# Kernel optimization log

Hardware: AMD Instinct MI355X
Metric: run time of the kernel (lower is better)

The kernel has to match this reference:

```python
import jax, jax.numpy as jnp
import numpy as np

# ---- config (mirrors init_kwargs) ----
R = 0.15          # ball-query radius
K = 32            # neighbors per ball
SP_STRIDE = 32    # spatial FPS stride
T_KERNEL = 3      # temporal tube length (odd)
T_STRIDE = 2
T_PAD = (1, 1)    # replicate padding
C0, C1 = 64, 128  # mlp_planes


def setup_inputs() -> dict:
    key = jax.random.key(0)
    k1, k2, k3 = jax.random.split(key, 3)
    B, T, N = 4, 32, 4096
    xyzs = jax.random.uniform(k1, (B, T, N, 3), dtype=jnp.float32)
    # 1x1 conv weights (no bias, no BN): conv_d: 4 -> C0, mlp: C0 -> C1
    Wd = jax.random.normal(k2, (C0, 4), dtype=jnp.float32) * (1.0 / np.sqrt(4))
    Wm = jax.random.normal(k3, (C1, C0), dtype=jnp.float32) * (1.0 / np.sqrt(C0))
    return {"xyzs": xyzs, "Wd": Wd, "Wm": Wm}


def _fps(xyz, m):
    """Furthest point sampling. xyz: (G,N,3) -> (G,m) int32, first index = 0."""
    G, N, _ = xyz.shape
    def step(carry, _):
        dist, last = carry                                   # (G,N), (G,)
        p = jnp.take_along_axis(xyz, last[:, None, None], axis=1)  # (G,1,3)
        d = jnp.sum((xyz - p) ** 2, axis=-1)                 # (G,N)
        dist = jnp.minimum(dist, d)
        nxt = jnp.argmax(dist, axis=-1).astype(jnp.int32)
        return (dist, nxt), nxt
    init = (jnp.full((G, N), 1e10, dtype=xyz.dtype), jnp.zeros((G,), jnp.int32))
    _, nxts = jax.lax.scan(step, init, None, length=m - 1)   # (m-1, G)
    return jnp.concatenate([jnp.zeros((G, 1), jnp.int32), jnp.swapaxes(nxts, 0, 1)], axis=1)


def _ball_query(r, k, neighbor_xyz, anchor_xyz):
    """First-k-within-radius, invalid slots filled with first valid (PointNet++ semantics).
    neighbor: (G,N,3), anchor: (G,M,3) -> idx (G,M,k) int32."""
    N = neighbor_xyz.shape[1]
    d2 = jnp.sum((anchor_xyz[:, :, None, :] - neighbor_xyz[:, None, :, :]) ** 2, axis=-1)  # (G,M,N)
    score = jnp.where(d2 < r * r, jnp.arange(N, dtype=jnp.int32), N)
    neg_topk, _ = jax.lax.top_k(-score, k)   # k smallest scores (ascending point index)
    idx = -neg_topk                          # (G,M,k)
    first = idx[..., :1]
    first = jnp.where(first == N, 0, first)
    return jnp.where(idx == N, first, idx)


def _group(pts, idx):
    """pts: (G,N,C), idx: (G,M,k) -> (G,M,k,C)."""
    G, M, k = idx.shape
    flat = jnp.take_along_axis(pts, idx.reshape(G, M * k)[..., None], axis=1)
    return flat.reshape(G, M, k, pts.shape[-1])


def _forward(xyzs, Wd, Wm):
    B, T, N, _ = xyzs.shape
    # replicate temporal padding
    xyz_pad = jnp.concatenate([xyzs[:, :1]] * T_PAD[0] + [xyzs] + [xyzs[:, -1:]] * T_PAD[1], axis=1)
    Tp = T + T_PAD[0] + T_PAD[1]
    half = T_KERNEL // 2
    ts = half + T_STRIDE * np.arange((Tp - T_KERNEL) // T_STRIDE + 1)  # output frame centers
    F = len(ts)
    M = N // SP_STRIDE

    center = xyz_pad[:, ts].reshape(B * F, N, 3)          # (G,N,3)
    anchor_idx = _fps(center, M)                          # (G,M)
    anchor = jnp.take_along_axis(center, anchor_idx[..., None], axis=1)  # (G,M,3)

    feat_sum = None
    for dt in range(-half, half + 1):                     # temporal tube (len 3)
        neigh = xyz_pad[:, ts + dt].reshape(B * F, N, 3)
        idx = _ball_query(R, K, neigh, anchor)            # (G,M,K)
        grouped = _group(neigh, idx)                      # (G,M,K,3)
        disp = grouped - anchor[:, :, None, :]
        tchan = jnp.full(disp.shape[:-1] + (1,), float(dt), dtype=disp.dtype)
        d4 = jnp.concatenate([disp, tchan], axis=-1)      # (G,M,K,4)
        h = jax.nn.relu(jnp.einsum('gmkc,oc->gmko', d4, Wd))   # conv_d + ReLU
        h = jax.nn.relu(jnp.einsum('gmki,oi->gmko', h, Wm))    # mlp + ReLU
        feat = jnp.max(h, axis=2)                         # spatial max pool over K -> (G,M,C1)
        feat_sum = feat if feat_sum is None else feat_sum + feat  # temporal sum pool

    new_xyzs = anchor.reshape(B, F, M, 3)
    new_features = jnp.transpose(feat_sum.reshape(B, F, M, C1), (0, 1, 3, 2))  # (B,F,C1,M)
    return new_xyzs, new_features


def reference(xyzs, Wd, Wm):
    return _forward(xyzs, Wd, Wm)
```

## Files before the change

kernel.cpp:

```cpp
#include <hip/hip_runtime.h>
#include <stdint.h>

#define B_   4
#define T_   32
#define N_   4096
#define F_   16
#define G_   64
#define M_   128
#define K_   32
#define C0_  64
#define C1_  128

typedef short  short8 __attribute__((ext_vector_type(8)));
typedef float  f32x4  __attribute__((ext_vector_type(4)));

static __device__ __forceinline__ short f2bf(float x) {
    union { float f; unsigned u; } v; v.f = x;
    unsigned r = (v.u + 0x7FFFu + ((v.u >> 16) & 1u)) >> 16;
    return (short)r;
}
static __device__ __forceinline__ float bf2f(short h) {
    union { float f; unsigned u; } v; v.u = ((unsigned)(unsigned short)h) << 16;
    return v.f;
}

template<int CTRL>
static __device__ __forceinline__ unsigned long long dpp_u64(unsigned long long v) {
    int lo = __builtin_amdgcn_update_dpp(0, (int)(unsigned)v,         CTRL, 0xF, 0xF, false);
    int hi = __builtin_amdgcn_update_dpp(0, (int)(unsigned)(v >> 32), CTRL, 0xF, 0xF, false);
    return ((unsigned long long)(unsigned)hi << 32) | (unsigned)lo;
}

__global__ __launch_bounds__(256) void fps_kernel(const float* __restrict__ xyzs,
                                                  float* __restrict__ anchors,
                                                  float* __restrict__ out_xyz,
                                                  const float* __restrict__ Wm,
                                                  short* __restrict__ Bhi_g,
                                                  short* __restrict__ Blo_g)
{
#pragma clang fp contract(off)
    if (blockIdx.x >= G_) {
        int id = (blockIdx.x - G_) * 256 + threadIdx.x;
        int o = id >> 3, c = id & 7;
        const float* wp = Wm + o * C0_ + c * 8;
        short8 hv, lv;
#pragma unroll
        for (int e = 0; e < 8; ++e) {
            float v = wp[e];
            short h = f2bf(v);
            short l = f2bf(v - bf2f(h));
            hv[e] = h; lv[e] = l;
        }
        int dst = o * C0_ + c * 8;
        *reinterpret_cast<short8*>(&Bhi_g[dst]) = hv;
        *reinterpret_cast<short8*>(&Blo_g[dst]) = lv;
        return;
    }

    const int g = blockIdx.x;
    const int b = g >> 4, f = g & 15;
    const float* base = xyzs + ((size_t)(b * T_ + 2 * f) * N_) * 3;
    const int t = threadIdx.x;
    const int wid = t >> 6;

    __shared__ unsigned long long skey[2][4];
    __shared__ float4 scrd[2][4];

    float x[16], y[16], z[16], dist[16];
#pragma unroll
    for (int j = 0; j < 16; ++j) {
        int p = j * 256 + t;
        x[j] = base[p * 3 + 0];
        y[j] = base[p * 3 + 1];
        z[j] = base[p * 3 + 2];
        dist[j] = 1e10f;
    }

    float px = base[0], py = base[1], pz = base[2];
    float rx = 0.f, ry = 0.f, rz = 0.f;
    if (t == 0) { rx = px; ry = py; rz = pz; }

    for (int it = 1; it < M_; ++it) {
        float bd = -1.0f; int bi = 0;
#pragma unroll
        for (int j = 0; j < 16; ++j) {
            float dx = x[j] - px;
            float dy = y[j] - py;
            float dz = z[j] - pz;
            float d = dx * dx + dy * dy;
            d = d + dz * dz;
            float nd = fminf(dist[j], d);
            dist[j] = nd;
            if (nd > bd) { bd = nd; bi = j * 256 + t; }
        }
        unsigned long long mykey =
            ((unsigned long long)__float_as_uint(bd) << 32) | (unsigned)(N_ - 1 - bi);
        unsigned long long key = mykey, k2;
        k2 = dpp_u64<0xB1>(key);  key = (k2 > key) ? k2 : key;
        k2 = dpp_u64<0x4E>(key);  key = (k2 > key) ? k2 : key;
        k2 = dpp_u64<0x124>(key); key = (k2 > key) ? k2 : key;
        k2 = dpp_u64<0x128>(key); key = (k2 > key) ? k2 : key;
        k2 = __shfl_xor(key, 16); key = (k2 > key) ? k2 : key;
        k2 = __shfl_xor(key, 32); key = (k2 > key) ? k2 : key;
        const int par = it & 1;
        if (mykey == key) {
            float wx = x[0], wy = y[0], wz = z[0];
#pragma unroll
            for (int j = 1; j < 16; ++j) {
                if (bi == j * 256 + t) { wx = x[j]; wy = y[j]; wz = z[j]; }
            }
            skey[par][wid] = key;
            scrd[par][wid] = make_float4(wx, wy, wz, 0.f);
        }
        __syncthreads();
        unsigned long long ck = skey[par][0];
        float4 cc = scrd[par][0];
#pragma unroll
        for (int w = 1; w < 4; ++w) {
            unsigned long long ok = skey[par][w];
            float4 oc = scrd[par][w];
            if (ok > ck) { ck = ok; cc = oc; }
        }
        px = cc.x; py = cc.y; pz = cc.z;
        if (t == it) { rx = px; ry = py; rz = pz; }
    }

    if (t < M_) {
        size_t ao = ((size_t)g * M_ + t) * 3;
        anchors[ao + 0] = rx; anchors[ao + 1] = ry; anchors[ao + 2] = rz;
        out_xyz[ao + 0] = rx; out_xyz[ao + 1] = ry; out_xyz[ao + 2] = rz;
    }
}

__global__ __launch_bounds__(256) void ballq_kernel(const float* __restrict__ xyzs,
                                                    const float* __restrict__ anchors,
                                                    int* __restrict__ widx)
{
#pragma clang fp contract(off)
    const float R2 = 0.0225f;
    const int wave = (blockIdx.x << 2) + (threadIdx.x >> 6);
    const int lane = threadIdx.x & 63;
    const int m   = wave % M_;
    const int gd  = wave / M_;
    const int dti = gd % 3;
    const int g   = gd / 3;
    const int b = g >> 4, f = g & 15;
    int tn = 2 * f + dti - 1;
    if (tn < 0) tn = 0;
    const float* nb = xyzs + ((size_t)(b * T_ + tn) * N_) * 3;
    const float* aw = anchors + ((size_t)g * M_ + m) * 3;
    const float ax = aw[0], ay = aw[1], az = aw[2];

    __shared__ int sbuf[4][K_];
    int* buf = sbuf[threadIdx.x >> 6];
    const unsigned long long lanebit = 1ULL << lane;

    int filled = 0;
    for (int cb = 0; cb < 8 && filled < K_; ++cb) {
        unsigned long long mk[8];
#pragma unroll
        for (int u = 0; u < 8; ++u) {
            int p = cb * 512 + u * 64 + lane;
            float dx = nb[p * 3 + 0] - ax;
            float dy = nb[p * 3 + 1] - ay;
            float dz = nb[p * 3 + 2] - az;
            float d2 = dx * dx + dy * dy;
            d2 = d2 + dz * dz;
            mk[u] = __ballot(d2 < R2);
        }
#pragma unroll
        for (int u = 0; u < 8; ++u) {
            if (mk[u] & lanebit) {
                int slot = filled + __popcll(mk[u] & (lanebit - 1ULL));
                if (slot < K_) buf[slot] = cb * 512 + u * 64 + lane;
            }
            filled += __popcll(mk[u]);
        }
    }
    __syncthreads();
    if (lane < K_) {
        int first = (filled > 0) ? buf[0] : 0;
        int v = (lane < filled) ? buf[lane] : first;
        widx[(size_t)wave * K_ + lane] = v;
    }
}

__global__ __launch_bounds__(256, 2) void mlp_kernel(const float* __restrict__ xyzs,
                                                     const float* __restrict__ Wd,
                                                     const short* __restrict__ Bhi_g,
                                                     const short* __restrict__ Blo_g,
                                                     const float* __restrict__ anchors,
                                                     const int* __restrict__ widx,
                                                     float* __restrict__ out_feat)
{
    const int t   = threadIdx.x;
    const int blk = blockIdx.x;
    const int g   = blk >> 6;
    const int m0  = (blk & 63) * 2;
    const int b = g >> 4, f = g & 15;

    const int lane = t & 63;
    const int w    = t >> 6;
    const int wml  = w & 1;
    const int wn   = w >> 1;
    const int row0 = lane & 15;
    const int kg   = lane >> 4;

    __shared__ __align__(16) short Ahi[192 * C0_];
    __shared__ float wd_s[C0_ * 4];
    __shared__ float pmf[2][C1_];

    short8 bh[4][2], bl[4][2];
#pragma unroll
    for (int nt = 0; nt < 4; ++nt) {
        int o = wn * 64 + nt * 16 + row0;
#pragma unroll
        for (int ks = 0; ks < 2; ++ks) {
            int off = o * C0_ + (ks * 4 + kg) * 8;
            bh[nt][ks] = *reinterpret_cast<const short8*>(&Bhi_g[off]);
            bl[nt][ks] = *reinterpret_cast<const short8*>(&Blo_g[off]);
        }
    }

    wd_s[t] = Wd[t];

    float dx = 0.f, dy = 0.f, dz = 0.f, dt4 = 0.f;
    if (t < 192) {
        int ml  = (t >= 96) ? 1 : 0;
        int rr  = t - ml * 96;
        int dti = rr >> 5, k = rr & 31;
        int m   = m0 + ml;
        int tn  = 2 * f + dti - 1;
        if (tn < 0) tn = 0;
        const float* nb = xyzs + ((size_t)(b * T_ + tn) * N_) * 3;
        int idx = widx[((size_t)(g * 3 + dti) * M_ + m) * K_ + k];
        const float* aw = anchors + ((size_t)g * M_ + m) * 3;
        dx = nb[idx * 3 + 0] - aw[0];
        dy = nb[idx * 3 + 1] - aw[1];
        dz = nb[idx * 3 + 2] - aw[2];
        dt4 = (float)(dti - 1);
    }
    __syncthreads();

    if (t < 192) {
#pragma unroll
        for (int u = 0; u < 8; ++u) {
            short8 hv;
#pragma unroll
            for (int e = 0; e < 8; ++e) {
                float4 wv = *reinterpret_cast<const float4*>(&wd_s[(u * 8 + e) * 4]);
                float s = dx * wv.x + dy * wv.y + dz * wv.z + dt4 * wv.w;
                hv[e] = f2bf(fmaxf(s, 0.0f));
            }
            *reinterpret_cast<short8*>(&Ahi[t * C0_ + ((u ^ (t & 7)) << 3)]) = hv;
        }
    }
    __syncthreads();

    f32x4 acc[6][4];
#pragma unroll
    for (int mt = 0; mt < 6; ++mt)
#pragma unroll
        for (int nt = 0; nt < 4; ++nt) {
            acc[mt][nt][0] = 0.f; acc[mt][nt][1] = 0.f;
            acc[mt][nt][2] = 0.f; acc[mt][nt][3] = 0.f;
        }

#pragma unroll
    for (int ks = 0; ks < 2; ++ks) {
        int chunk = ks * 4 + kg;
        short8 ah[6];
#pragma unroll
        for (int mt = 0; mt < 6; ++mt) {
            int r = wml * 96 + mt * 16 + row0;
            ah[mt] = *reinterpret_cast<const short8*>(&Ahi[r * C0_ + ((chunk ^ (r & 7)) << 3)]);
        }
#pragma unroll
        for (int mt = 0; mt < 6; ++mt)
#pragma unroll
            for (int nt = 0; nt < 4; ++nt) {
                acc[mt][nt] = __builtin_amdgcn_mfma_f32_16x16x32_bf16(ah[mt], bh[nt][ks], acc[mt][nt], 0, 0, 0);
                acc[mt][nt] = __builtin_amdgcn_mfma_f32_16x16x32_bf16(ah[mt], bl[nt][ks], acc[mt][nt], 0, 0, 0);
            }
    }

#pragma unroll
    for (int nt = 0; nt < 4; ++nt) {
        float fs = 0.f;
#pragma unroll
        for (int dti = 0; dti < 3; ++dti) {
            f32x4 a0 = acc[dti * 2 + 0][nt];
            f32x4 a1 = acc[dti * 2 + 1][nt];
            float mv = fmaxf(fmaxf(fmaxf(a0[0], a0[1]), fmaxf(a0[2], a0[3])),
                             fmaxf(fmaxf(a1[0], a1[1]), fmaxf(a1[2], a1[3])));
            mv = fmaxf(mv, 0.0f);
            mv = fmaxf(mv, __shfl_xor(mv, 16));
            mv = fmaxf(mv, __shfl_xor(mv, 32));
            fs += mv;
        }
        if (lane < 16) pmf[wml][wn * 64 + nt * 16 + lane] = fs;
    }
    __syncthreads();

    if (t < C1_) {
        float2 v = make_float2(pmf[0][t], pmf[1][t]);
        *reinterpret_cast<float2*>(&out_feat[((size_t)g * C1_ + t) * M_ + m0]) = v;
    }
}

extern "C" void kernel_launch(void* const* d_in, const int* in_sizes, int n_in,
                              void* d_out, int out_size, void* d_ws, size_t ws_size,
                              hipStream_t stream)
{
    (void)in_sizes; (void)n_in; (void)out_size; (void)ws_size;
    const float* xyzs = (const float*)d_in[0];
    const float* Wd   = (const float*)d_in[1];
    const float* Wm   = (const float*)d_in[2];
    float* out = (float*)d_out;

    char* ws = (char*)d_ws;
    short* Bhi_g   = (short*)ws;
    short* Blo_g   = (short*)(ws + 16384);
    float* anchors = (float*)(ws + 32768);
    int*   widx    = (int*)(ws + 32768 + (size_t)G_ * M_ * 3 * 4);

    float* out_xyz  = out;
    float* out_feat = out + G_ * M_ * 3;

    hipLaunchKernelGGL(fps_kernel,    dim3(G_ + 4),           dim3(256), 0, stream,
                       xyzs, anchors, out_xyz, Wm, Bhi_g, Blo_g);
    hipLaunchKernelGGL(ballq_kernel,  dim3(G_ * 3 * M_ / 4),  dim3(256), 0, stream, xyzs, anchors, widx);
    hipLaunchKernelGGL(mlp_kernel,    dim3(G_ * 64),          dim3(256), 0, stream,
                       xyzs, Wd, Bhi_g, Blo_g, anchors, widx, out_feat);
}
```

Before: 316.4 us.

## Widen FPS blocks to 1024 threads and carry coordinates through DPP reductions

The furthest-point-sampling kernel now runs with 1024 threads per block, so each thread holds 4 points instead of 16. That shortens the serial per-iteration distance update in a kernel that launches only 64 blocks. The argmax reduction now carries the winning point's coordinates through the DPP lane exchanges, using row_bcast steps instead of shuffles. This removes the post-reduction coordinate lookup. The cross-wave step reduces 16 wave results with DPP instead of a serial loop over 4, which adds more synchronization and reduction work per iteration in exchange.

```diff
diff --git a/kernel.cpp b/kernel.cpp
--- a/kernel.cpp
+++ b/kernel.cpp
@@ -30,17 +30,31 @@
     int hi = __builtin_amdgcn_update_dpp(0, (int)(unsigned)(v >> 32), CTRL, 0xF, 0xF, false);
     return ((unsigned long long)(unsigned)hi << 32) | (unsigned)lo;
 }
-
-__global__ __launch_bounds__(256) void fps_kernel(const float* __restrict__ xyzs,
-                                                  float* __restrict__ anchors,
-                                                  float* __restrict__ out_xyz,
-                                                  const float* __restrict__ Wm,
-                                                  short* __restrict__ Bhi_g,
-                                                  short* __restrict__ Blo_g)
+template<int CTRL>
+static __device__ __forceinline__ float dpp_f32(float v) {
+    return __int_as_float(__builtin_amdgcn_update_dpp(0, __float_as_int(v), CTRL, 0xF, 0xF, false));
+}
+
+template<int CTRL>
+static __device__ __forceinline__ void dpp_combine(unsigned long long& key,
+                                                   float& cx, float& cy, float& cz) {
+    unsigned long long k2 = dpp_u64<CTRL>(key);
+    float ox = dpp_f32<CTRL>(cx);
+    float oy = dpp_f32<CTRL>(cy);
+    float oz = dpp_f32<CTRL>(cz);
+    if (k2 > key) { key = k2; cx = ox; cy = oy; cz = oz; }
+}
+
+__global__ __launch_bounds__(1024) void fps_kernel(const float* __restrict__ xyzs,
+                                                   float* __restrict__ anchors,
+                                                   float* __restrict__ out_xyz,
+                                                   const float* __restrict__ Wm,
+                                                   short* __restrict__ Bhi_g,
+                                                   short* __restrict__ Blo_g)
 {
 #pragma clang fp contract(off)
     if (blockIdx.x >= G_) {
-        int id = (blockIdx.x - G_) * 256 + threadIdx.x;
+        int id = threadIdx.x;
         int o = id >> 3, c = id & 7;
         const float* wp = Wm + o * C0_ + c * 8;
         short8 hv, lv;
@@ -61,15 +75,16 @@
     const int b = g >> 4, f = g & 15;
     const float* base = xyzs + ((size_t)(b * T_ + 2 * f) * N_) * 3;
     const int t = threadIdx.x;
+    const int lane = t & 63;
     const int wid = t >> 6;
 
-    __shared__ unsigned long long skey[2][4];
-    __shared__ float4 scrd[2][4];
-
-    float x[16], y[16], z[16], dist[16];
-#pragma unroll
-    for (int j = 0; j < 16; ++j) {
-        int p = j * 256 + t;
+    __shared__ unsigned long long skey[2][16];
+    __shared__ __align__(16) float4 scrd[2][16];
+
+    float x[4], y[4], z[4], dist[4];
+#pragma unroll
+    for (int j = 0; j < 4; ++j) {
+        int p = j * 1024 + t;
         x[j] = base[p * 3 + 0];
         y[j] = base[p * 3 + 1];
         z[j] = base[p * 3 + 2];
@@ -83,7 +98,7 @@
     for (int it = 1; it < M_; ++it) {
         float bd = -1.0f; int bi = 0;
 #pragma unroll
-        for (int j = 0; j < 16; ++j) {
+        for (int j = 0; j < 4; ++j) {
             float dx = x[j] - px;
             float dy = y[j] - py;
             float dz = z[j] - pz;
@@ -91,37 +106,35 @@
             d = d + dz * dz;
             float nd = fminf(dist[j], d);
             dist[j] = nd;
-            if (nd > bd) { bd = nd; bi = j * 256 + t; }
-        }
-        unsigned long long mykey =
+            if (nd > bd) { bd = nd; bi = j * 1024 + t; }
+        }
+        unsigned long long key =
             ((unsigned long long)__float_as_uint(bd) << 32) | (unsigned)(N_ - 1 - bi);
-        unsigned long long key = mykey, k2;
-        k2 = dpp_u64<0xB1>(key);  key = (k2 > key) ? k2 : key;
-        k2 = dpp_u64<0x4E>(key);  key = (k2 > key) ? k2 : key;
-        k2 = dpp_u64<0x124>(key); key = (k2 > key) ? k2 : key;
-        k2 = dpp_u64<0x128>(key); key = (k2 > key) ? k2 : key;
-        k2 = __shfl_xor(key, 16); key = (k2 > key) ? k2 : key;
-        k2 = __shfl_xor(key, 32); key = (k2 > key) ? k2 : key;
+        float cx = x[0], cy = y[0], cz = z[0];
+#pragma unroll
+        for (int j = 1; j < 4; ++j) {
+            if (bi == j * 1024 + t) { cx = x[j]; cy = y[j]; cz = z[j]; }
+        }
+        dpp_combine<0xB1>(key, cx, cy, cz);
+        dpp_combine<0x4E>(key, cx, cy, cz);
+        dpp_combine<0x124>(key, cx, cy, cz);
+        dpp_combine<0x128>(key, cx, cy, cz);
+        dpp_combine<0x142>(key, cx, cy, cz);
+        dpp_combine<0x143>(key, cx, cy, cz);
         const int par = it & 1;
-        if (mykey == key) {
-            float wx = x[0], wy = y[0], wz = z[0];
-#pragma unroll
-            for (int j = 1; j < 16; ++j) {
-                if (bi == j * 256 + t) { wx = x[j]; wy = y[j]; wz = z[j]; }
-            }
+        if (lane == 63) {
             skey[par][wid] = key;
-            scrd[par][wid] = make_float4(wx, wy, wz, 0.f);
+            scrd[par][wid] = make_float4(cx, cy, cz, 0.f);
         }
         __syncthreads();
-        unsigned long long ck = skey[par][0];
-        float4 cc = scrd[par][0];
-#pragma unroll
-        for (int w = 1; w < 4; ++w) {
-            unsigned long long ok = skey[par][w];
-            float4 oc = scrd[par][w];
-            if (ok > ck) { ck = ok; cc = oc; }
-        }
-        px = cc.x; py = cc.y; pz = cc.z;
+        unsigned long long ck = skey[par][lane & 15];
+        float4 cc4 = scrd[par][lane & 15];
+        float kx = cc4.x, ky = cc4.y, kz = cc4.z;
+        dpp_combine<0xB1>(ck, kx, ky, kz);
+        dpp_combine<0x4E>(ck, kx, ky, kz);
+        dpp_combine<0x124>(ck, kx, ky, kz);
+        dpp_combine<0x128>(ck, kx, ky, kz);
+        px = kx; py = ky; pz = kz;
         if (t == it) { rx = px; ry = py; rz = pz; }
     }
 
@@ -327,7 +340,7 @@
     float* out_xyz  = out;
     float* out_feat = out + G_ * M_ * 3;
 
-    hipLaunchKernelGGL(fps_kernel,    dim3(G_ + 4),           dim3(256), 0, stream,
+    hipLaunchKernelGGL(fps_kernel,    dim3(G_ + 1),           dim3(1024), 0, stream,
                        xyzs, anchors, out_xyz, Wm, Bhi_g, Blo_g);
     hipLaunchKernelGGL(ballq_kernel,  dim3(G_ * 3 * M_ / 4),  dim3(256), 0, stream, xyzs, anchors, widx);
     hipLaunchKernelGGL(mlp_kernel,    dim3(G_ * 64),          dim3(256), 0, stream,
```

Result: slower. 359.6 us (+13.7%).
